# Performance work log

Hardware: AMD Instinct MI355X
Metric: run time of the kernel (lower is better)

## Reference

```python
import jax, jax.numpy as jnp
import numpy as np
from math import sqrt

IN_DIM = 512
OUT_DIM = 512
MOD_DIM = 256
BATCH = 1024
EPS = 1e-8


def _uniform_param(key, shape, fan_in):
    # torch.rand in [0,1) then scaled to [-k, k) with k = sqrt(1/fan_in)
    k = sqrt(1.0 / fan_in)
    return jax.random.uniform(key, shape, dtype=jnp.float32, minval=-k, maxval=k)


def setup_inputs() -> dict:
    key = jax.random.key(0)
    k1, k2, k3, k4, k5, k6 = jax.random.split(key, 6)
    modulations = jax.random.normal(k1, (BATCH, MOD_DIM), dtype=jnp.float32)
    x = jax.random.normal(k2, (BATCH, IN_DIM), dtype=jnp.float32)
    weight = _uniform_param(k3, (OUT_DIM, IN_DIM), IN_DIM)      # main weight
    bias = _uniform_param(k4, (OUT_DIM,), IN_DIM)               # main bias
    # nn.Linear(modulation_dim, in_dim): weight [in_dim, mod_dim], bias [in_dim]
    mod_w = _uniform_param(k5, (IN_DIM, MOD_DIM), MOD_DIM)
    mod_b = _uniform_param(k6, (IN_DIM,), MOD_DIM)
    return {"modulations": modulations, "x": x, "weight": weight,
            "bias": bias, "mod_w": mod_w, "mod_b": mod_b}


def reference(modulations, x, weight, bias, mod_w, mod_b):
    # scales: [B, in_dim]
    scales = modulations @ mod_w.T + mod_b
    # weight_1: [B, out_dim, in_dim] = weight broadcast-scaled per sample
    w1 = weight[None, :, :] * scales[:, None, :]
    # NOTE: faithful to source: sum over axis -2 (the OUT dim), per-column L2 renorm
    w2 = w1 * jax.lax.rsqrt(jnp.sum(jnp.square(w1), axis=-2, keepdims=True) + EPS)
    # (x.unsqueeze(-2) @ w2.transpose(-2,-1)).squeeze(-2) + bias -> [B, out_dim]
    out = jnp.einsum("bi,boi->bo", x, w2) + bias
    return out
```

## Files before the change

### kernel.cpp

```cpp
#include <hip/hip_runtime.h>
#include <math.h>

#define B_DIM    1024
#define IN_DIMS  512
#define OUT_DIMS 512
#define MOD_DIM  256
#define EPS_F    1e-8f

typedef __attribute__((ext_vector_type(8))) short bf16x8;
typedef __attribute__((ext_vector_type(4))) float f32x4;

__device__ __forceinline__ unsigned short f2bf(float f) {
    union { float f; unsigned u; } c; c.f = f;
    unsigned r = c.u + 0x7fffu + ((c.u >> 16) & 1u);
    return (unsigned short)(r >> 16);
}
__device__ __forceinline__ float bf2f(unsigned short h) {
    union { float f; unsigned u; } c; c.u = ((unsigned)h) << 16;
    return c.f;
}

#define LP1 264
__global__ __launch_bounds__(256) void k1_mod(
    const float* __restrict__ mods,
    const float* __restrict__ mod_w,
    const float* __restrict__ mod_b,
    const float* __restrict__ weight,
    const float* __restrict__ x,
    unsigned short* __restrict__ t_bf)
{
    __shared__ unsigned short Ah[32 * LP1], Al[32 * LP1];
    __shared__ unsigned short Bh[64 * LP1], Bl[64 * LP1];
    __shared__ float4 csm[16][16];
    __shared__ float colsum_s[64];

    const int tid = threadIdx.x;
    const int n0 = blockIdx.x * 64;
    const int m0 = blockIdx.y * 32;
    const int lane = tid & 63, wv = tid >> 6;
    const int wm = (wv >> 1) * 16, wn = (wv & 1) * 32;
    const int lr = lane & 15, lq = lane >> 4;

    #pragma unroll
    for (int i = 0; i < 8; i++) {
        const int id = tid + i * 256;
        const int r = id >> 6, c4 = id & 63;
        float4 v = *(const float4*)&mods[(m0 + r) * MOD_DIM + c4 * 4];
        ushort4 h, l;
        h.x = f2bf(v.x); l.x = f2bf(v.x - bf2f(h.x));
        h.y = f2bf(v.y); l.y = f2bf(v.y - bf2f(h.y));
        h.z = f2bf(v.z); l.z = f2bf(v.z - bf2f(h.z));
        h.w = f2bf(v.w); l.w = f2bf(v.w - bf2f(h.w));
        *(ushort4*)&Ah[r * LP1 + c4 * 4] = h;
        *(ushort4*)&Al[r * LP1 + c4 * 4] = l;
    }
    #pragma unroll
    for (int i = 0; i < 16; i++) {
        const int id = tid + i * 256;
        const int r = id >> 6, c4 = id & 63;
        float4 v = *(const float4*)&mod_w[(n0 + r) * MOD_DIM + c4 * 4];
        ushort4 h, l;
        h.x = f2bf(v.x); l.x = f2bf(v.x - bf2f(h.x));
        h.y = f2bf(v.y); l.y = f2bf(v.y - bf2f(h.y));
        h.z = f2bf(v.z); l.z = f2bf(v.z - bf2f(h.z));
        h.w = f2bf(v.w); l.w = f2bf(v.w - bf2f(h.w));
        *(ushort4*)&Bh[r * LP1 + c4 * 4] = h;
        *(ushort4*)&Bl[r * LP1 + c4 * 4] = l;
    }

    {
        const int c4 = tid & 15, rr = tid >> 4;
        float4 acc = {0.f, 0.f, 0.f, 0.f};
        #pragma unroll
        for (int it = 0; it < 32; it++) {
            const int row = rr + 16 * it;
            float4 v = *(const float4*)&weight[row * IN_DIMS + n0 + c4 * 4];
            acc.x += v.x * v.x; acc.y += v.y * v.y;
            acc.z += v.z * v.z; acc.w += v.w * v.w;
        }
        csm[rr][c4] = acc;
    }
    __syncthreads();
    if (tid < 16) {
        float4 s = csm[0][tid];
        #pragma unroll
        for (int j = 1; j < 16; j++) {
            float4 v = csm[j][tid];
            s.x += v.x; s.y += v.y; s.z += v.z; s.w += v.w;
        }
        *(float4*)&colsum_s[tid * 4] = s;
    }

    f32x4 acc[2] = {};
    #pragma unroll
    for (int kk = 0; kk < 256; kk += 32) {
        const int ko = kk + lq * 8;
        bf16x8 ah = *(bf16x8*)&Ah[(wm + lr) * LP1 + ko];
        bf16x8 al = *(bf16x8*)&Al[(wm + lr) * LP1 + ko];
        bf16x8 bh0 = *(bf16x8*)&Bh[(wn +      lr) * LP1 + ko];
        bf16x8 bh1 = *(bf16x8*)&Bh[(wn + 16 + lr) * LP1 + ko];
        bf16x8 bl0 = *(bf16x8*)&Bl[(wn +      lr) * LP1 + ko];
        bf16x8 bl1 = *(bf16x8*)&Bl[(wn + 16 + lr) * LP1 + ko];
        acc[0] = __builtin_amdgcn_mfma_f32_16x16x32_bf16(ah, bh0, acc[0], 0, 0, 0);
        acc[1] = __builtin_amdgcn_mfma_f32_16x16x32_bf16(ah, bh1, acc[1], 0, 0, 0);
        acc[0] = __builtin_amdgcn_mfma_f32_16x16x32_bf16(ah, bl0, acc[0], 0, 0, 0);
        acc[1] = __builtin_amdgcn_mfma_f32_16x16x32_bf16(ah, bl1, acc[1], 0, 0, 0);
        acc[0] = __builtin_amdgcn_mfma_f32_16x16x32_bf16(al, bh0, acc[0], 0, 0, 0);
        acc[1] = __builtin_amdgcn_mfma_f32_16x16x32_bf16(al, bh1, acc[1], 0, 0, 0);
    }
    __syncthreads();

    #pragma unroll
    for (int j = 0; j < 2; j++) {
        const int ln = wn + 16 * j + lr;
        const int gn = n0 + ln;
        const float cs = colsum_s[ln];
        const float mb = mod_b[gn];
        #pragma unroll
        for (int rr = 0; rr < 4; rr++) {
            const int gm = m0 + wm + lq * 4 + rr;
            const float s = acc[j][rr] + mb;
            const float tv = x[gm * IN_DIMS + gn] * s * rsqrtf(s * s * cs + EPS_F);
            t_bf[gm * IN_DIMS + gn] = f2bf(tv);
        }
    }
}

#define LP2 536
__global__ __launch_bounds__(256) void k2_out(
    const unsigned short* __restrict__ t_bf,
    const float* __restrict__ weight,
    const float* __restrict__ bias,
    float* __restrict__ out)
{
    __shared__ unsigned short As[32 * LP2];
    __shared__ unsigned short Bs[64 * LP2];

    const int tid = threadIdx.x;
    const int n0 = blockIdx.x * 64;
    const int m0 = blockIdx.y * 32;
    const int lane = tid & 63, wv = tid >> 6;
    const int wm = (wv >> 1) * 16, wn = (wv & 1) * 32;
    const int lr = lane & 15, lq = lane >> 4;

    #pragma unroll
    for (int i = 0; i < 8; i++) {
        const int id = tid + i * 256;
        const int r = id >> 6, c8 = id & 63;
        *(uint4*)&As[r * LP2 + c8 * 8] =
            *(const uint4*)&t_bf[(m0 + r) * IN_DIMS + c8 * 8];
    }
    #pragma unroll
    for (int i = 0; i < 32; i++) {
        const int id = tid + i * 256;
        const int r = id >> 7, c4 = id & 127;
        float4 v = *(const float4*)&weight[(n0 + r) * IN_DIMS + c4 * 4];
        ushort4 h;
        h.x = f2bf(v.x); h.y = f2bf(v.y); h.z = f2bf(v.z); h.w = f2bf(v.w);
        *(ushort4*)&Bs[r * LP2 + c4 * 4] = h;
    }
    __syncthreads();

    f32x4 acc[2] = {};
    #pragma unroll
    for (int kk = 0; kk < 512; kk += 32) {
        const int ko = kk + lq * 8;
        bf16x8 a  = *(bf16x8*)&As[(wm + lr) * LP2 + ko];
        bf16x8 b0 = *(bf16x8*)&Bs[(wn +      lr) * LP2 + ko];
        bf16x8 b1 = *(bf16x8*)&Bs[(wn + 16 + lr) * LP2 + ko];
        acc[0] = __builtin_amdgcn_mfma_f32_16x16x32_bf16(a, b0, acc[0], 0, 0, 0);
        acc[1] = __builtin_amdgcn_mfma_f32_16x16x32_bf16(a, b1, acc[1], 0, 0, 0);
    }

    #pragma unroll
    for (int j = 0; j < 2; j++) {
        const int gn = n0 + wn + 16 * j + lr;
        const float bv = bias[gn];
        #pragma unroll
        for (int rr = 0; rr < 4; rr++) {
            const int gm = m0 + wm + lq * 4 + rr;
            out[gm * OUT_DIMS + gn] = acc[j][rr] + bv;
        }
    }
}

extern "C" void kernel_launch(void* const* d_in, const int* in_sizes, int n_in,
                              void* d_out, int out_size, void* d_ws, size_t ws_size,
                              hipStream_t stream)
{
    const float* modulations = (const float*)d_in[0];
    const float* x           = (const float*)d_in[1];
    const float* weight      = (const float*)d_in[2];
    const float* bias        = (const float*)d_in[3];
    const float* mod_w       = (const float*)d_in[4];
    const float* mod_b       = (const float*)d_in[5];
    float* out = (float*)d_out;

    unsigned short* t_bf = (unsigned short*)d_ws;

    k1_mod<<<dim3(8, 32), 256, 0, stream>>>(
        modulations, mod_w, mod_b, weight, x, t_bf);

    k2_out<<<dim3(8, 32), 256, 0, stream>>>(
        t_bf, weight, bias, out);
}
```

Baseline: 77.44 us.

## Fuse modulation and output GEMM kernels via cooperative grid sync

Merges the two kernels into one cooperative kernel that runs the scale/normalize GEMM, performs a grid-wide sync, then runs the output GEMM while reusing a single aliased shared-memory buffer. The aim is to remove the second launch and the gap between kernels. In exchange it relies on all 256 blocks being co-resident, and the grid barrier adds its own cost. The larger static shared allocation (about 103 KB) also limits occupancy.

Measured after the change: 114.3 us. +47.6%, slower.

```diff
diff --git a/kernel.cpp b/kernel.cpp
--- a/kernel.cpp
+++ b/kernel.cpp
@@ -1,4 +1,5 @@
 #include <hip/hip_runtime.h>
+#include <hip/hip_cooperative_groups.h>
 #include <math.h>
 
 #define B_DIM    1024
@@ -7,32 +8,44 @@
 #define MOD_DIM  256
 #define EPS_F    1e-8f
 
+#define LPB 264
+#define LPC 520
+
 typedef __attribute__((ext_vector_type(8))) short bf16x8;
 typedef __attribute__((ext_vector_type(4))) float f32x4;
-
-__device__ __forceinline__ unsigned short f2bf(float f) {
+typedef unsigned short ush;
+
+namespace cg = cooperative_groups;
+
+__device__ __forceinline__ ush f2bf(float f) {
     union { float f; unsigned u; } c; c.f = f;
     unsigned r = c.u + 0x7fffu + ((c.u >> 16) & 1u);
-    return (unsigned short)(r >> 16);
-}
-__device__ __forceinline__ float bf2f(unsigned short h) {
+    return (ush)(r >> 16);
+}
+__device__ __forceinline__ float bf2f(ush h) {
     union { float f; unsigned u; } c; c.u = ((unsigned)h) << 16;
     return c.f;
 }
 
-#define LP1 264
-__global__ __launch_bounds__(256) void k1_mod(
+__global__ __launch_bounds__(256) void fused_all(
     const float* __restrict__ mods,
+    const float* __restrict__ x,
+    const float* __restrict__ weight,
+    const float* __restrict__ bias,
     const float* __restrict__ mod_w,
     const float* __restrict__ mod_b,
-    const float* __restrict__ weight,
-    const float* __restrict__ x,
-    unsigned short* __restrict__ t_bf)
+    ush* __restrict__ t_bf,
+    float* __restrict__ out)
 {
-    __shared__ unsigned short Ah[32 * LP1], Al[32 * LP1];
-    __shared__ unsigned short Bh[64 * LP1], Bl[64 * LP1];
-    __shared__ float4 csm[16][16];
-    __shared__ float colsum_s[64];
+    __shared__ __align__(16) char smem[105728];
+    ush* Ah = (ush*)smem;
+    ush* Al = Ah + 32 * LPB;
+    ush* Bh = Al + 32 * LPB;
+    ush* Bl = Bh + 64 * LPB;
+    float4* csm    = (float4*)(smem + 101376);
+    float*  colsum = (float*)(smem + 105472);
+    ush* As = (ush*)smem;
+    ush* Bs = As + 32 * LPC;
 
     const int tid = threadIdx.x;
     const int n0 = blockIdx.x * 64;
@@ -51,8 +64,8 @@
         h.y = f2bf(v.y); l.y = f2bf(v.y - bf2f(h.y));
         h.z = f2bf(v.z); l.z = f2bf(v.z - bf2f(h.z));
         h.w = f2bf(v.w); l.w = f2bf(v.w - bf2f(h.w));
-        *(ushort4*)&Ah[r * LP1 + c4 * 4] = h;
-        *(ushort4*)&Al[r * LP1 + c4 * 4] = l;
+        *(ushort4*)&Ah[r * LPB + c4 * 4] = h;
+        *(ushort4*)&Al[r * LPB + c4 * 4] = l;
     }
     #pragma unroll
     for (int i = 0; i < 16; i++) {
@@ -64,10 +77,9 @@
         h.y = f2bf(v.y); l.y = f2bf(v.y - bf2f(h.y));
         h.z = f2bf(v.z); l.z = f2bf(v.z - bf2f(h.z));
         h.w = f2bf(v.w); l.w = f2bf(v.w - bf2f(h.w));
-        *(ushort4*)&Bh[r * LP1 + c4 * 4] = h;
-        *(ushort4*)&Bl[r * LP1 + c4 * 4] = l;
-    }
-
+        *(ushort4*)&Bh[r * LPB + c4 * 4] = h;
+        *(ushort4*)&Bl[r * LPB + c4 * 4] = l;
+    }
     {
         const int c4 = tid & 15, rr = tid >> 4;
         float4 acc = {0.f, 0.f, 0.f, 0.f};
@@ -78,29 +90,29 @@
             acc.x += v.x * v.x; acc.y += v.y * v.y;
             acc.z += v.z * v.z; acc.w += v.w * v.w;
         }
-        csm[rr][c4] = acc;
+        csm[rr * 16 + c4] = acc;
     }
     __syncthreads();
     if (tid < 16) {
-        float4 s = csm[0][tid];
+        float4 s = csm[tid];
         #pragma unroll
         for (int j = 1; j < 16; j++) {
-            float4 v = csm[j][tid];
+            float4 v = csm[j * 16 + tid];
             s.x += v.x; s.y += v.y; s.z += v.z; s.w += v.w;
         }
-        *(float4*)&colsum_s[tid * 4] = s;
+        *(float4*)&colsum[tid * 4] = s;
     }
 
     f32x4 acc[2] = {};
     #pragma unroll
     for (int kk = 0; kk < 256; kk += 32) {
         const int ko = kk + lq * 8;
-        bf16x8 ah = *(bf16x8*)&Ah[(wm + lr) * LP1 + ko];
-        bf16x8 al = *(bf16x8*)&Al[(wm + lr) * LP1 + ko];
-        bf16x8 bh0 = *(bf16x8*)&Bh[(wn +      lr) * LP1 + ko];
-        bf16x8 bh1 = *(bf16x8*)&Bh[(wn + 16 + lr) * LP1 + ko];
-        bf16x8 bl0 = *(bf16x8*)&Bl[(wn +      lr) * LP1 + ko];
-        bf16x8 bl1 = *(bf16x8*)&Bl[(wn + 16 + lr) * LP1 + ko];
+        bf16x8 ah  = *(bf16x8*)&Ah[(wm + lr) * LPB + ko];
+        bf16x8 al  = *(bf16x8*)&Al[(wm + lr) * LPB + ko];
+        bf16x8 bh0 = *(bf16x8*)&Bh[(wn +      lr) * LPB + ko];
+        bf16x8 bh1 = *(bf16x8*)&Bh[(wn + 16 + lr) * LPB + ko];
+        bf16x8 bl0 = *(bf16x8*)&Bl[(wn +      lr) * LPB + ko];
+        bf16x8 bl1 = *(bf16x8*)&Bl[(wn + 16 + lr) * LPB + ko];
         acc[0] = __builtin_amdgcn_mfma_f32_16x16x32_bf16(ah, bh0, acc[0], 0, 0, 0);
         acc[1] = __builtin_amdgcn_mfma_f32_16x16x32_bf16(ah, bh1, acc[1], 0, 0, 0);
         acc[0] = __builtin_amdgcn_mfma_f32_16x16x32_bf16(ah, bl0, acc[0], 0, 0, 0);
@@ -114,7 +126,7 @@
     for (int j = 0; j < 2; j++) {
         const int ln = wn + 16 * j + lr;
         const int gn = n0 + ln;
-        const float cs = colsum_s[ln];
+        const float cs = colsum[ln];
         const float mb = mod_b[gn];
         #pragma unroll
         for (int rr = 0; rr < 4; rr++) {
@@ -124,30 +136,14 @@
             t_bf[gm * IN_DIMS + gn] = f2bf(tv);
         }
     }
-}
-
-#define LP2 536
-__global__ __launch_bounds__(256) void k2_out(
-    const unsigned short* __restrict__ t_bf,
-    const float* __restrict__ weight,
-    const float* __restrict__ bias,
-    float* __restrict__ out)
-{
-    __shared__ unsigned short As[32 * LP2];
-    __shared__ unsigned short Bs[64 * LP2];
-
-    const int tid = threadIdx.x;
-    const int n0 = blockIdx.x * 64;
-    const int m0 = blockIdx.y * 32;
-    const int lane = tid & 63, wv = tid >> 6;
-    const int wm = (wv >> 1) * 16, wn = (wv & 1) * 32;
-    const int lr = lane & 15, lq = lane >> 4;
+
+    cg::this_grid().sync();
 
     #pragma unroll
     for (int i = 0; i < 8; i++) {
         const int id = tid + i * 256;
         const int r = id >> 6, c8 = id & 63;
-        *(uint4*)&As[r * LP2 + c8 * 8] =
+        *(uint4*)&As[r * LPC + c8 * 8] =
             *(const uint4*)&t_bf[(m0 + r) * IN_DIMS + c8 * 8];
     }
     #pragma unroll
@@ -157,19 +153,19 @@
         float4 v = *(const float4*)&weight[(n0 + r) * IN_DIMS + c4 * 4];
         ushort4 h;
         h.x = f2bf(v.x); h.y = f2bf(v.y); h.z = f2bf(v.z); h.w = f2bf(v.w);
-        *(ushort4*)&Bs[r * LP2 + c4 * 4] = h;
+        *(ushort4*)&Bs[r * LPC + c4 * 4] = h;
     }
     __syncthreads();
 
-    f32x4 acc[2] = {};
+    f32x4 acc2[2] = {};
     #pragma unroll
     for (int kk = 0; kk < 512; kk += 32) {
         const int ko = kk + lq * 8;
-        bf16x8 a  = *(bf16x8*)&As[(wm + lr) * LP2 + ko];
-        bf16x8 b0 = *(bf16x8*)&Bs[(wn +      lr) * LP2 + ko];
-        bf16x8 b1 = *(bf16x8*)&Bs[(wn + 16 + lr) * LP2 + ko];
-        acc[0] = __builtin_amdgcn_mfma_f32_16x16x32_bf16(a, b0, acc[0], 0, 0, 0);
-        acc[1] = __builtin_amdgcn_mfma_f32_16x16x32_bf16(a, b1, acc[1], 0, 0, 0);
+        bf16x8 a  = *(bf16x8*)&As[(wm + lr) * LPC + ko];
+        bf16x8 b0 = *(bf16x8*)&Bs[(wn +      lr) * LPC + ko];
+        bf16x8 b1 = *(bf16x8*)&Bs[(wn + 16 + lr) * LPC + ko];
+        acc2[0] = __builtin_amdgcn_mfma_f32_16x16x32_bf16(a, b0, acc2[0], 0, 0, 0);
+        acc2[1] = __builtin_amdgcn_mfma_f32_16x16x32_bf16(a, b1, acc2[1], 0, 0, 0);
     }
 
     #pragma unroll
@@ -179,7 +175,7 @@
         #pragma unroll
         for (int rr = 0; rr < 4; rr++) {
             const int gm = m0 + wm + lq * 4 + rr;
-            out[gm * OUT_DIMS + gn] = acc[j][rr] + bv;
+            out[gm * OUT_DIMS + gn] = acc2[j][rr] + bv;
         }
     }
 }
@@ -195,12 +191,12 @@
     const float* mod_w       = (const float*)d_in[4];
     const float* mod_b       = (const float*)d_in[5];
     float* out = (float*)d_out;
-
-    unsigned short* t_bf = (unsigned short*)d_ws;
-
-    k1_mod<<<dim3(8, 32), 256, 0, stream>>>(
-        modulations, mod_w, mod_b, weight, x, t_bf);
-
-    k2_out<<<dim3(8, 32), 256, 0, stream>>>(
-        t_bf, weight, bias, out);
-}
+    ush* t_bf = (ush*)d_ws;
+
+    void* args[] = {
+        (void*)&modulations, (void*)&x, (void*)&weight, (void*)&bias,
+        (void*)&mod_w, (void*)&mod_b, (void*)&t_bf, (void*)&out
+    };
+    hipLaunchCooperativeKernel((const void*)fused_all, dim3(8, 32), dim3(256),
+                               args, 0, stream);
+}
```
